# Optimization experiments

Hardware: AMD Instinct MI355X
Metric: run time of the kernel (lower is better)

## Reference

```python
import jax, jax.numpy as jnp
import numpy as np

NUM_NOTES = 88
ALPHA = 0.3  # smoothing_strength
EPS = 1e-8


def _init_transition_logits(n=NUM_NOTES):
    # Faithful vectorization of _init_musical_priors (conditions checked in order).
    i = np.arange(n)[:, None]
    j = np.arange(n)[None, :]
    iv = np.abs(i - j)
    logits = np.select(
        [iv == 0, iv <= 2, iv <= 5, iv == 7, iv == 12],
        [3.0, 2.0, 1.0, 1.5, 1.0],
        default=-1.0,
    ).astype(np.float32)
    return jnp.asarray(logits)


def setup_inputs() -> dict:
    key = jax.random.key(0)
    frame_logits = jax.random.normal(key, (64, 4000, NUM_NOTES), dtype=jnp.float32)
    return {"frame_logits": frame_logits, "transition_logits": _init_transition_logits()}


def reference(frame_logits, transition_logits):
    # frame_logits: (B, T, N); transition_logits: (N, N)
    trans_probs = jax.nn.softmax(transition_logits, axis=1)          # (N, N)
    cur_probs = jax.nn.softmax(frame_logits, axis=-1)                # (B, T, N)
    first = frame_logits[:, 0, :]                                    # (B, N)

    def step(prev_smoothed, cur_p):
        prev_probs = jax.nn.softmax(prev_smoothed, axis=-1)          # (B, N)
        expected_next = prev_probs @ trans_probs                     # (B, N)
        blended = ALPHA * expected_next + (1.0 - ALPHA) * cur_p
        out = jnp.log(blended + EPS)
        return out, out

    xs = jnp.swapaxes(cur_probs[:, 1:, :], 0, 1)                     # (T-1, B, N)
    _, rest = jax.lax.scan(step, first, xs)                          # (T-1, B, N)
    rest = jnp.swapaxes(rest, 0, 1)                                  # (B, T-1, N)
    return jnp.concatenate([first[:, None, :], rest], axis=1)       # (B, T, N)
```

## Files before the change

kernel.cpp:

```cpp
#include <hip/hip_runtime.h>
#include <math.h>

#define NOTES 88
#define TSTEPS 4000
#define NCHUNK 250
#define LEN 16
#define WARMD 8
#define EPSV 1e-8f
#define PSTR 100

typedef __attribute__((ext_vector_type(8))) short short8;
typedef __attribute__((ext_vector_type(4))) float f32x4;

__device__ __forceinline__ unsigned cvt_pk_bf16(float lo, float hi) {
    unsigned r;
    asm("v_cvt_pk_bf16_f32 %0, %1, %2" : "=v"(r) : "v"(lo), "v"(hi));
    return r;
}

__device__ __forceinline__ float hsum4(float s) {
    s += __shfl_xor(s, 16);
    s += __shfl_xor(s, 32);
    return s;
}

__global__ __launch_bounds__(64, 1)
void fused_scan(const float* __restrict__ f, const float* __restrict__ T,
                float* __restrict__ out) {
    const int l = threadIdx.x;
    const int m = l & 15, hi = l >> 4;
    const int c = (int)(blockIdx.x % NCHUNK);
    const int bg = (int)(blockIdx.x / NCHUNK);
    const int b = bg * 16 + m;

    __shared__ float sM[96], sI[96];
    __shared__ unsigned short pls[16 * PSTR];

    for (int r = l; r < NOTES; r += 64) {
        const float4* row = (const float4*)(T + r * NOTES);
        float4 v[22];
#pragma unroll
        for (int q = 0; q < 22; ++q) v[q] = row[q];
        float mx = -1e30f;
#pragma unroll
        for (int q = 0; q < 22; ++q)
            mx = fmaxf(mx, fmaxf(fmaxf(v[q].x, v[q].y), fmaxf(v[q].z, v[q].w)));
        float s = 0.f;
#pragma unroll
        for (int q = 0; q < 22; ++q)
            s += __expf(v[q].x - mx) + __expf(v[q].y - mx) +
                 __expf(v[q].z - mx) + __expf(v[q].w - mx);
        sM[r] = mx;
        sI[r] = 1.0f / s;
    }
    __syncthreads();

    short8 Af[6][3];
#pragma unroll
    for (int nt = 0; nt < 6; ++nt) {
        const int n = nt * 16 + m;
#pragma unroll
        for (int kt = 0; kt < 3; ++kt) {
            float v[8];
#pragma unroll
            for (int e = 0; e < 8; ++e) {
                const int k = kt * 32 + hi * 8 + e;
                float val = 0.f;
                if (k < NOTES && n < NOTES)
                    val = __expf(T[k * NOTES + n] - sM[k]) * sI[k];
                v[e] = val;
            }
            union { unsigned u[4]; short8 s8; } uu;
#pragma unroll
            for (int q = 0; q < 4; ++q) uu.u[q] = cvt_pk_bf16(v[2 * q], v[2 * q + 1]);
            Af[nt][kt] = uu.s8;
        }
    }

    const int t0 = LEN * c;
    const int tend = t0 + LEN;
    const int tfirst = (c == 0) ? 0 : t0 - WARMD;

    const float* fb = f + (size_t)b * TSTEPS * NOTES;
    float* ob = out + (size_t)b * TSTEPS * NOTES;
    const bool padq = (80 + 4 * hi) >= NOTES;
    unsigned short* pbase = pls + m * PSTR;

    auto loadRow = [&](int t, float4 (&rv)[6]) {
        const float4* rp = (const float4*)(fb + (size_t)t * NOTES);
#pragma unroll
        for (int nt = 0; nt < 6; ++nt) {
            int idx = 4 * nt + hi;
            if (nt == 5 && padq) idx = 0;
            rv[nt] = rp[idx];
        }
        if (padq) { rv[5].x = -1e30f; rv[5].y = -1e30f; rv[5].z = -1e30f; rv[5].w = -1e30f; }
    };

    auto softmaxRow = [&](const float4 (&rv)[6], float4 (&cp)[6]) {
        float s = 0.f;
#pragma unroll
        for (int nt = 0; nt < 6; ++nt) {
            cp[nt].x = __expf(rv[nt].x);
            cp[nt].y = __expf(rv[nt].y);
            cp[nt].z = __expf(rv[nt].z);
            cp[nt].w = __expf(rv[nt].w);
            s += cp[nt].x + cp[nt].y + cp[nt].z + cp[nt].w;
        }
        s = hsum4(s);
        const float inv = 1.0f / s;
#pragma unroll
        for (int nt = 0; nt < 6; ++nt) {
            cp[nt].x *= inv; cp[nt].y *= inv; cp[nt].z *= inv; cp[nt].w *= inv;
        }
    };

    auto writeP = [&](const float4 (&p)[6]) {
#pragma unroll
        for (int nt = 0; nt < 6; ++nt) {
            uint2 w;
            w.x = cvt_pk_bf16(p[nt].x, p[nt].y);
            w.y = cvt_pk_bf16(p[nt].z, p[nt].w);
            *(uint2*)(pbase + 16 * nt + 4 * hi) = w;
        }
    };

    short8 Bf[3];
    auto readB = [&]() {
#pragma unroll
        for (int kt = 0; kt < 3; ++kt)
            Bf[kt] = *(const short8*)(pbase + 32 * kt + 8 * hi);
    };

    auto stepS = [&](float4 (&row)[6], int t, bool store) {
        float4 cp[6];
        softmaxRow(row, cp);
        {
            const int tp = t + 4;
            if (tp < tend) loadRow(tp, row);
        }
        f32x4 acc[6];
#pragma unroll
        for (int nt = 0; nt < 6; ++nt) acc[nt] = (f32x4){0.f, 0.f, 0.f, 0.f};
#pragma unroll
        for (int kt = 0; kt < 3; ++kt) {
#pragma unroll
            for (int nt = 0; nt < 6; ++nt)
                acc[nt] = __builtin_amdgcn_mfma_f32_16x16x32_bf16(
                    Af[nt][kt], Bf[kt], acc[nt], 0, 0, 0);
        }
        float4 x[6];
#pragma unroll
        for (int nt = 0; nt < 6; ++nt) {
            x[nt].x = fmaf(0.3f, acc[nt][0], fmaf(0.7f, cp[nt].x, EPSV));
            x[nt].y = fmaf(0.3f, acc[nt][1], fmaf(0.7f, cp[nt].y, EPSV));
            x[nt].z = fmaf(0.3f, acc[nt][2], fmaf(0.7f, cp[nt].z, EPSV));
            x[nt].w = fmaf(0.3f, acc[nt][3], fmaf(0.7f, cp[nt].w, EPSV));
        }
        writeP(x);
        readB();
        if (store) {
#pragma unroll
            for (int nt = 0; nt < 6; ++nt) {
                if (nt == 5 && padq) continue;
                float4 o;
                o.x = __logf(x[nt].x);
                o.y = __logf(x[nt].y);
                o.z = __logf(x[nt].z);
                o.w = __logf(x[nt].w);
                *(float4*)(ob + (size_t)t * NOTES + 16 * nt + 4 * hi) = o;
            }
        }
    };

    float4 R0[6], R1[6], R2[6], R3[6];
    loadRow(tfirst, R0);
    loadRow(tfirst + 1, R1);
    loadRow(tfirst + 2, R2);
    loadRow(tfirst + 3, R3);

    {
        float4 cp[6];
        softmaxRow(R0, cp);
        if (c == 0) {
#pragma unroll
            for (int nt = 0; nt < 6; ++nt)
                if (!(nt == 5 && padq))
                    *(float4*)(ob + 16 * nt + 4 * hi) = R0[nt];
        }
        loadRow(tfirst + 4, R0);
        writeP(cp);
        readB();
    }

    const bool st0 = (c == 0);
    stepS(R1, tfirst + 1, st0);
    stepS(R2, tfirst + 2, st0);
    stepS(R3, tfirst + 3, st0);

    int t = tfirst + 4;
    if (c != 0) {
        stepS(R0, t + 0, false);
        stepS(R1, t + 1, false);
        stepS(R2, t + 2, false);
        stepS(R3, t + 3, false);
        t += 4;
    }
    while (t < tend) {
        stepS(R0, t + 0, true);
        stepS(R1, t + 1, true);
        stepS(R2, t + 2, true);
        stepS(R3, t + 3, true);
        t += 4;
    }
}

extern "C" void kernel_launch(void* const* d_in, const int* in_sizes, int n_in,
                              void* d_out, int out_size, void* d_ws, size_t ws_size,
                              hipStream_t stream) {
    const float* f = (const float*)d_in[0];
    const float* T = (const float*)d_in[1];
    float* out = (float*)d_out;
    const int batch = in_sizes[0] / (TSTEPS * NOTES);
    const int blocks = (batch / 16) * NCHUNK;
    fused_scan<<<blocks, 64, 0, stream>>>(f, T, out);
}
```

Baseline: 63.43 us.

## Interleave two independent time chunks per wave and stage outputs through LDS

Each wave now processes two independent 8-step chunks, A and B, in lockstep. Their MFMA, softmax and LDS round-trip chains interleave to hide the latency of the serial recurrence. Output log-probabilities are staged in shared memory two timesteps at a time and flushed with coalesced nontemporal row stores, replacing the earlier scattered per-lane stores. Chunk length halves, so the warmup overhead per stored step doubles. The change also adds LDS usage and more registers held by the pair of chunks.

```diff
diff --git a/kernel.cpp b/kernel.cpp
--- a/kernel.cpp
+++ b/kernel.cpp
@@ -3,11 +3,12 @@
 
 #define NOTES 88
 #define TSTEPS 4000
-#define NCHUNK 250
-#define LEN 16
+#define LEN 8
+#define KPB 250
 #define WARMD 8
 #define EPSV 1e-8f
 #define PSTR 100
+#define OSTR 180
 
 typedef __attribute__((ext_vector_type(8))) short short8;
 typedef __attribute__((ext_vector_type(4))) float f32x4;
@@ -29,12 +30,14 @@
                 float* __restrict__ out) {
     const int l = threadIdx.x;
     const int m = l & 15, hi = l >> 4;
-    const int c = (int)(blockIdx.x % NCHUNK);
-    const int bg = (int)(blockIdx.x / NCHUNK);
+    const int kA = (int)(blockIdx.x % KPB);
+    const int kB = kA + KPB;
+    const int bg = (int)(blockIdx.x / KPB);
     const int b = bg * 16 + m;
 
     __shared__ float sM[96], sI[96];
-    __shared__ unsigned short pls[16 * PSTR];
+    __shared__ unsigned short plsA[16 * PSTR], plsB[16 * PSTR];
+    __shared__ float soA[16 * OSTR], soB[16 * OSTR];
 
     for (int r = l; r < NOTES; r += 64) {
         const float4* row = (const float4*)(T + r * NOTES);
@@ -77,14 +80,17 @@
         }
     }
 
-    const int t0 = LEN * c;
-    const int tend = t0 + LEN;
-    const int tfirst = (c == 0) ? 0 : t0 - WARMD;
+    const int t0A = LEN * kA, tendA = t0A + LEN;
+    const int tfA = (kA == 0) ? 0 : t0A - WARMD;
+    const int tstoreA = (kA == 0) ? 1 : t0A;
+    const int t0B = LEN * kB, tendB = t0B + LEN;
+    const int tfB = t0B - WARMD;
+    const int tstoreB = t0B;
 
     const float* fb = f + (size_t)b * TSTEPS * NOTES;
-    float* ob = out + (size_t)b * TSTEPS * NOTES;
     const bool padq = (80 + 4 * hi) >= NOTES;
-    unsigned short* pbase = pls + m * PSTR;
+    unsigned short* pbA = plsA + m * PSTR;
+    unsigned short* pbB = plsB + m * PSTR;
 
     auto loadRow = [&](int t, float4 (&rv)[6]) {
         const float4* rp = (const float4*)(fb + (size_t)t * NOTES);
@@ -115,7 +121,7 @@
         }
     };
 
-    auto writeP = [&](const float4 (&p)[6]) {
+    auto writeP = [&](unsigned short* pbase, const float4 (&p)[6]) {
 #pragma unroll
         for (int nt = 0; nt < 6; ++nt) {
             uint2 w;
@@ -125,20 +131,27 @@
         }
     };
 
-    short8 Bf[3];
-    auto readB = [&]() {
+    short8 BfA[3], BfB[3];
+    auto readB = [&](unsigned short* pbase, short8 (&Bf)[3]) {
 #pragma unroll
         for (int kt = 0; kt < 3; ++kt)
             Bf[kt] = *(const short8*)(pbase + 32 * kt + 8 * hi);
     };
 
-    auto stepS = [&](float4 (&row)[6], int t, bool store) {
-        float4 cp[6];
-        softmaxRow(row, cp);
-        {
-            const int tp = t + 4;
-            if (tp < tend) loadRow(tp, row);
-        }
+    auto flushG = [&](float* soc, int tg) {
+        float* obase0 = out + (size_t)(bg * 16) * TSTEPS * NOTES + (size_t)tg * NOTES;
+#pragma unroll 4
+        for (int mm = 0; mm < 16; ++mm) {
+            if (l < 44) {
+                const f32x4 v0 = *(const f32x4*)&soc[mm * OSTR + 4 * l];
+                __builtin_nontemporal_store(
+                    v0, (f32x4*)(obase0 + (size_t)mm * TSTEPS * NOTES) + l);
+            }
+        }
+    };
+
+    auto mfmaBlend = [&](const short8 (&Bf)[3], const float4 (&cp)[6],
+                         float4 (&x)[6]) {
         f32x4 acc[6];
 #pragma unroll
         for (int nt = 0; nt < 6; ++nt) acc[nt] = (f32x4){0.f, 0.f, 0.f, 0.f};
@@ -149,7 +162,6 @@
                 acc[nt] = __builtin_amdgcn_mfma_f32_16x16x32_bf16(
                     Af[nt][kt], Bf[kt], acc[nt], 0, 0, 0);
         }
-        float4 x[6];
 #pragma unroll
         for (int nt = 0; nt < 6; ++nt) {
             x[nt].x = fmaf(0.3f, acc[nt][0], fmaf(0.7f, cp[nt].x, EPSV));
@@ -157,9 +169,13 @@
             x[nt].z = fmaf(0.3f, acc[nt][2], fmaf(0.7f, cp[nt].z, EPSV));
             x[nt].w = fmaf(0.3f, acc[nt][3], fmaf(0.7f, cp[nt].w, EPSV));
         }
-        writeP(x);
-        readB();
-        if (store) {
+    };
+
+    auto tail = [&](const float4 (&x)[6], int t, int t0c, int tstorec,
+                    int tendc, float* soc) {
+        if (t >= tstorec && t < tendc) {
+            const int tm = (t - t0c) & 1;
+            float* sb = soc + m * OSTR + tm * 88;
 #pragma unroll
             for (int nt = 0; nt < 6; ++nt) {
                 if (nt == 5 && padq) continue;
@@ -168,50 +184,64 @@
                 o.y = __logf(x[nt].y);
                 o.z = __logf(x[nt].z);
                 o.w = __logf(x[nt].w);
-                *(float4*)(ob + (size_t)t * NOTES + 16 * nt + 4 * hi) = o;
+                *(float4*)(sb + 16 * nt + 4 * hi) = o;
             }
-        }
-    };
-
-    float4 R0[6], R1[6], R2[6], R3[6];
-    loadRow(tfirst, R0);
-    loadRow(tfirst + 1, R1);
-    loadRow(tfirst + 2, R2);
-    loadRow(tfirst + 3, R3);
+            if (tm == 1) flushG(soc, t - 1);
+        }
+    };
 
     {
-        float4 cp[6];
-        softmaxRow(R0, cp);
-        if (c == 0) {
+        float4 r0[6], cp[6];
+        loadRow(tfA, r0);
+        softmaxRow(r0, cp);
+        if (kA == 0) {
+            float* sb = soA + m * OSTR;
 #pragma unroll
             for (int nt = 0; nt < 6; ++nt)
                 if (!(nt == 5 && padq))
-                    *(float4*)(ob + 16 * nt + 4 * hi) = R0[nt];
-        }
-        loadRow(tfirst + 4, R0);
-        writeP(cp);
-        readB();
-    }
-
-    const bool st0 = (c == 0);
-    stepS(R1, tfirst + 1, st0);
-    stepS(R2, tfirst + 2, st0);
-    stepS(R3, tfirst + 3, st0);
-
-    int t = tfirst + 4;
-    if (c != 0) {
-        stepS(R0, t + 0, false);
-        stepS(R1, t + 1, false);
-        stepS(R2, t + 2, false);
-        stepS(R3, t + 3, false);
-        t += 4;
-    }
-    while (t < tend) {
-        stepS(R0, t + 0, true);
-        stepS(R1, t + 1, true);
-        stepS(R2, t + 2, true);
-        stepS(R3, t + 3, true);
-        t += 4;
+                    *(float4*)(sb + 16 * nt + 4 * hi) = r0[nt];
+        }
+        writeP(pbA, cp);
+        readB(pbA, BfA);
+    }
+    {
+        float4 r0[6], cp[6];
+        loadRow(tfB, r0);
+        softmaxRow(r0, cp);
+        writeP(pbB, cp);
+        readB(pbB, BfB);
+    }
+
+    float4 A0[6], A1[6], A2[6], B0[6], B1[6], B2[6];
+    loadRow(tfA + 1, A0); loadRow(tfB + 1, B0);
+    loadRow(tfA + 2 < tendA ? tfA + 2 : tendA - 1, A1);
+    loadRow(tfB + 2, B1);
+
+    auto stepPair = [&](float4 (&curA)[6], float4 (&nxtA)[6],
+                        float4 (&curB)[6], float4 (&nxtB)[6],
+                        int tA, int tB) {
+        loadRow(tA + 2 < tendA ? tA + 2 : tendA - 1, nxtA);
+        loadRow(tB + 2 < tendB ? tB + 2 : tendB - 1, nxtB);
+        float4 cpA[6], cpB[6];
+        softmaxRow(curA, cpA);
+        softmaxRow(curB, cpB);
+        float4 xA[6], xB[6];
+        mfmaBlend(BfA, cpA, xA);
+        mfmaBlend(BfB, cpB, xB);
+        writeP(pbA, xA);
+        writeP(pbB, xB);
+        readB(pbA, BfA);
+        readB(pbB, BfB);
+        tail(xA, tA, t0A, tstoreA, tendA, soA);
+        tail(xB, tB, t0B, tstoreB, tendB, soB);
+    };
+
+#pragma unroll
+    for (int it = 0; it < 15; ++it) {
+        const int tA = tfA + 1 + it, tB = tfB + 1 + it;
+        if (it % 3 == 0)      stepPair(A0, A2, B0, B2, tA, tB);
+        else if (it % 3 == 1) stepPair(A1, A0, B1, B0, tA, tB);
+        else                  stepPair(A2, A1, B2, B1, tA, tB);
     }
 }
 
@@ -222,6 +252,6 @@
     const float* T = (const float*)d_in[1];
     float* out = (float*)d_out;
     const int batch = in_sizes[0] / (TSTEPS * NOTES);
-    const int blocks = (batch / 16) * NCHUNK;
+    const int blocks = (batch / 16) * KPB;
     fused_scan<<<blocks, 64, 0, stream>>>(f, T, out);
 }
```

After: 200.9 us. 217% more time.
